# Performance work log

Hardware: AMD Instinct MI355X
Metric: run time of the kernel (lower is better)

The kernel has to match this reference:

```python
import jax, jax.numpy as jnp
import numpy as np

NUM_PTS = 1024
LATENT_SIZE = 32
BETA = 0.1


def setup_inputs() -> dict:
    key = jax.random.key(0)
    k1, k2, k3, k4 = jax.random.split(key, 4)
    B = 128
    return {
        "recon_x": jax.random.normal(k1, (B, NUM_PTS, 3), dtype=jnp.float32),
        "x": jax.random.normal(k2, (B, NUM_PTS, 3), dtype=jnp.float32),
        "mu": jax.random.normal(k3, (B, LATENT_SIZE), dtype=jnp.float32),
        "logvar": jax.random.normal(k4, (B, LATENT_SIZE), dtype=jnp.float32),
    }


def _chamfer(recon_x, x):
    # Batched squared pairwise distances: P[b, i, j] = ||x[b,i] - recon_x[b,j]||^2
    xx = jnp.sum(x * x, axis=-1)              # [B, N]
    yy = jnp.sum(recon_x * recon_x, axis=-1)  # [B, N]
    xy = jnp.einsum("bnd,bmd->bnm", x, recon_x)  # [B, N, N]
    P = xx[:, :, None] + yy[:, None, :] - 2.0 * xy
    # Bidirectional min + sum
    loss_1 = jnp.sum(jnp.min(P, axis=1))  # for each recon point, nearest x point
    loss_2 = jnp.sum(jnp.min(P, axis=2))  # for each x point, nearest recon point
    return loss_1 + loss_2


def reference(recon_x, x, mu, logvar):
    RE = _chamfer(recon_x, x) / NUM_PTS
    KLD = -0.5 * jnp.sum(1.0 + logvar - mu * mu - jnp.exp(logvar))
    KLD = KLD / LATENT_SIZE
    return RE + KLD * BETA
```

## Files before the change

### kernel.cpp

```cpp
#include <hip/hip_runtime.h>

#define NUM_PTS 1024
#define NBATCH 128
#define BT 256
#define RT 256
#define NJC 8
#define JCH 64
#define R 16
#define CHAMF_SCALE (1.0f / 1024.0f)
#define KLD_SCALE   (-0.5f * 0.1f / 32.0f)

#define WS_CHUNK (NBATCH * NUM_PTS)
#define WS_DIR   (NJC * WS_CHUNK)

__global__ __launch_bounds__(BT, 4) void chamfer_part(
    const float* __restrict__ recon_x,
    const float* __restrict__ x,
    float* __restrict__ ws)
{
    const int b  = blockIdx.x & 127;
    const int c  = blockIdx.x >> 7;
    const int w  = threadIdx.x >> 6;
    const int lt = threadIdx.x & 63;
    const int dir  = w & 1;
    const int half = w >> 1;

    __shared__ float sq[4][4][JCH];
    __shared__ float comb[2][NUM_PTS + 64];

    {
        const float* qsrc = (dir == 0 ? recon_x : x)
            + (size_t)b * NUM_PTS * 3 + (size_t)(c * 128 + half * JCH + lt) * 3;
        const float qx = qsrc[0], qy = qsrc[1], qz = qsrc[2];
        sq[w][0][lt] = qx;
        sq[w][1][lt] = qy;
        sq[w][2][lt] = qz;
        sq[w][3][lt] = fmaf(qx, qx, fmaf(qy, qy, qz * qz));
    }

    const float* rp = (dir == 0 ? x : recon_x) + (size_t)b * NUM_PTS * 3;
    float vx[R], vy[R], vz[R], m[R];
    {
        float buf[48];
        const float4* __restrict__ s4 = (const float4*)(rp + 48 * lt);
        float4* bp = (float4*)buf;
#pragma unroll
        for (int i = 0; i < 12; ++i) bp[i] = s4[i];
#pragma unroll
        for (int k = 0; k < R; ++k) {
            vx[k] = -2.0f * buf[3 * k + 0];
            vy[k] = -2.0f * buf[3 * k + 1];
            vz[k] = -2.0f * buf[3 * k + 2];
            m[k]  = 1e30f;
        }
    }

    const float4* __restrict__ qxp = (const float4*)sq[w][0];
    const float4* __restrict__ qyp = (const float4*)sq[w][1];
    const float4* __restrict__ qzp = (const float4*)sq[w][2];
    const float4* __restrict__ q2p = (const float4*)sq[w][3];
#pragma unroll 2
    for (int g = 0; g < JCH / 4; ++g) {
        const float4 qx = qxp[g];
        const float4 qy = qyp[g];
        const float4 qz = qzp[g];
        const float4 q2 = q2p[g];
#pragma unroll
        for (int r = 0; r < R; ++r) {
            const float d0 = fmaf(vx[r], qx.x, fmaf(vy[r], qy.x, fmaf(vz[r], qz.x, q2.x)));
            const float d1 = fmaf(vx[r], qx.y, fmaf(vy[r], qy.y, fmaf(vz[r], qz.y, q2.y)));
            m[r] = fminf(fminf(m[r], d0), d1);
        }
#pragma unroll
        for (int r = 0; r < R; ++r) {
            const float d2 = fmaf(vx[r], qx.z, fmaf(vy[r], qy.z, fmaf(vz[r], qz.z, q2.z)));
            const float d3 = fmaf(vx[r], qx.w, fmaf(vy[r], qy.w, fmaf(vz[r], qz.w, q2.w)));
            m[r] = fminf(fminf(m[r], d2), d3);
        }
    }

    if (half == 0) {
#pragma unroll
        for (int k = 0; k < R; ++k)
            comb[dir][17 * lt + k] = m[k];
    }
    __syncthreads();
    if (half == 1) {
        float4* dst = (float4*)(ws + (size_t)dir * WS_DIR + (size_t)c * WS_CHUNK
                                + b * NUM_PTS + 16 * lt);
#pragma unroll
        for (int k4 = 0; k4 < 4; ++k4) {
            float o[4];
#pragma unroll
            for (int i = 0; i < 4; ++i) {
                const int k = 4 * k4 + i;
                const float mm = fminf(m[k], comb[dir][17 * lt + k]);
                const float r2 = 0.25f * fmaf(vx[k], vx[k],
                                        fmaf(vy[k], vy[k], vz[k] * vz[k]));
                o[i] = r2 + mm;
            }
            dst[k4] = make_float4(o[0], o[1], o[2], o[3]);
        }
    }
}

__global__ __launch_bounds__(RT) void reduce_kernel(
    const float* __restrict__ ws,
    const float* __restrict__ mu,
    const float* __restrict__ logvar,
    float* __restrict__ out)
{
    const int gid  = blockIdx.x * RT + threadIdx.x;
    const int base = gid * 4;
    const int dir  = base >> 17;
    const int rem  = base & 131071;

    const float4* p = (const float4*)(ws + (size_t)dir * WS_DIR + rem);
    float4 mn = p[0];
#pragma unroll
    for (int c = 1; c < NJC; ++c) {
        const float4 q = p[c * (WS_CHUNK / 4)];
        mn.x = fminf(mn.x, q.x);
        mn.y = fminf(mn.y, q.y);
        mn.z = fminf(mn.z, q.z);
        mn.w = fminf(mn.w, q.w);
    }
    float v = (mn.x + mn.y + mn.z + mn.w) * CHAMF_SCALE;

    if (blockIdx.x < 16) {
        const int t = blockIdx.x * RT + threadIdx.x;
        const float lv = logvar[t];
        const float mm = mu[t];
        v += (1.0f + lv - mm * mm - expf(lv)) * KLD_SCALE;
    }

    for (int off = 32; off > 0; off >>= 1)
        v += __shfl_down(v, off, 64);

    __shared__ float red[RT / 64];
    const int lane = threadIdx.x & 63;
    const int wv   = threadIdx.x >> 6;
    if (lane == 0) red[wv] = v;
    __syncthreads();
    if (threadIdx.x == 0) {
        float sum = 0.f;
        for (int wq = 0; wq < RT / 64; ++wq) sum += red[wq];
        atomicAdd(out, sum);
    }
}

extern "C" void kernel_launch(void* const* d_in, const int* in_sizes, int n_in,
                              void* d_out, int out_size, void* d_ws, size_t ws_size,
                              hipStream_t stream) {
    const float* recon_x = (const float*)d_in[0];
    const float* x       = (const float*)d_in[1];
    const float* mu      = (const float*)d_in[2];
    const float* logvar  = (const float*)d_in[3];
    float* out = (float*)d_out;
    float* ws  = (float*)d_ws;

    (void)hipMemsetAsync(out, 0, sizeof(float), stream);

    chamfer_part<<<NBATCH * NJC, BT, 0, stream>>>(recon_x, x, ws);
    reduce_kernel<<<256, RT, 0, stream>>>(ws, mu, logvar, out);
}
```

Measured before the change: 89.09 us.

## Fuse reduction into chamfer kernel via last-block-done atomic counters

Merges the separate reduction kernel into the chamfer kernel. Each batch's eighth finishing block reduces that batch's per-chunk minima plus its KLD slice, and the last batch block sums all per-batch partials into the output. This removes a kernel launch and its gap, at the cost of threadfences, atomic counters and a tail where a single block per batch does the reduction serially.

```diff
diff --git a/kernel.cpp b/kernel.cpp
--- a/kernel.cpp
+++ b/kernel.cpp
@@ -3,7 +3,6 @@
 #define NUM_PTS 1024
 #define NBATCH 128
 #define BT 256
-#define RT 256
 #define NJC 8
 #define JCH 64
 #define R 16
@@ -12,11 +11,15 @@
 
 #define WS_CHUNK (NBATCH * NUM_PTS)
 #define WS_DIR   (NJC * WS_CHUNK)
+#define WS_PART  (2 * WS_DIR)
 
-__global__ __launch_bounds__(BT, 4) void chamfer_part(
+__global__ __launch_bounds__(BT, 4) void fused_kernel(
     const float* __restrict__ recon_x,
     const float* __restrict__ x,
-    float* __restrict__ ws)
+    const float* __restrict__ mu,
+    const float* __restrict__ logvar,
+    float* __restrict__ ws,
+    float* __restrict__ out)
 {
     const int b  = blockIdx.x & 127;
     const int c  = blockIdx.x >> 7;
@@ -25,8 +28,13 @@
     const int dir  = w & 1;
     const int half = w >> 1;
 
+    int* const cnt    = (int*)(ws + WS_PART);
+    float* const bsum = ws + WS_PART + 256;
+
     __shared__ float sq[4][4][JCH];
     __shared__ float comb[2][NUM_PTS + 64];
+    __shared__ int   sflag;
+    __shared__ float red[BT / 64];
 
     {
         const float* qsrc = (dir == 0 ? recon_x : x)
@@ -102,51 +110,61 @@
             dst[k4] = make_float4(o[0], o[1], o[2], o[3]);
         }
     }
-}
 
-__global__ __launch_bounds__(RT) void reduce_kernel(
-    const float* __restrict__ ws,
-    const float* __restrict__ mu,
-    const float* __restrict__ logvar,
-    float* __restrict__ out)
-{
-    const int gid  = blockIdx.x * RT + threadIdx.x;
-    const int base = gid * 4;
-    const int dir  = base >> 17;
-    const int rem  = base & 131071;
+    __threadfence();
+    __syncthreads();
+    if (threadIdx.x == 0) sflag = atomicAdd(&cnt[b], 1);
+    __syncthreads();
+    if (sflag != 7) return;
 
-    const float4* p = (const float4*)(ws + (size_t)dir * WS_DIR + rem);
-    float4 mn = p[0];
+    __threadfence();
+    float v = 0.0f;
 #pragma unroll
-    for (int c = 1; c < NJC; ++c) {
-        const float4 q = p[c * (WS_CHUNK / 4)];
-        mn.x = fminf(mn.x, q.x);
-        mn.y = fminf(mn.y, q.y);
-        mn.z = fminf(mn.z, q.z);
-        mn.w = fminf(mn.w, q.w);
+    for (int gsel = 0; gsel < 2; ++gsel) {
+        const int grp  = threadIdx.x + BT * gsel;
+        const int rdir = grp >> 8;
+        const int rowg = grp & 255;
+        const float4* p = (const float4*)(ws + (size_t)rdir * WS_DIR
+                                          + (size_t)b * NUM_PTS) + rowg;
+        float4 mn = p[0];
+#pragma unroll
+        for (int cc = 1; cc < NJC; ++cc) {
+            const float4 q = p[cc * (WS_CHUNK / 4)];
+            mn.x = fminf(mn.x, q.x);
+            mn.y = fminf(mn.y, q.y);
+            mn.z = fminf(mn.z, q.z);
+            mn.w = fminf(mn.w, q.w);
+        }
+        v += mn.x + mn.y + mn.z + mn.w;
     }
-    float v = (mn.x + mn.y + mn.z + mn.w) * CHAMF_SCALE;
-
-    if (blockIdx.x < 16) {
-        const int t = blockIdx.x * RT + threadIdx.x;
+    v *= CHAMF_SCALE;
+    if (threadIdx.x < 32) {
+        const int t = b * 32 + threadIdx.x;
         const float lv = logvar[t];
         const float mm = mu[t];
         v += (1.0f + lv - mm * mm - expf(lv)) * KLD_SCALE;
     }
-
     for (int off = 32; off > 0; off >>= 1)
         v += __shfl_down(v, off, 64);
-
-    __shared__ float red[RT / 64];
-    const int lane = threadIdx.x & 63;
-    const int wv   = threadIdx.x >> 6;
-    if (lane == 0) red[wv] = v;
+    if ((threadIdx.x & 63) == 0) red[threadIdx.x >> 6] = v;
     __syncthreads();
     if (threadIdx.x == 0) {
-        float sum = 0.f;
-        for (int wq = 0; wq < RT / 64; ++wq) sum += red[wq];
-        atomicAdd(out, sum);
+        float s = red[0] + red[1] + red[2] + red[3];
+        bsum[b] = s;
+        __threadfence();
+        sflag = atomicAdd(&cnt[128], 1);
     }
+    __syncthreads();
+    if (sflag != 127) return;
+
+    __threadfence();
+    float f = (threadIdx.x < 128) ? bsum[threadIdx.x] : 0.0f;
+    for (int off = 32; off > 0; off >>= 1)
+        f += __shfl_down(f, off, 64);
+    if ((threadIdx.x & 63) == 0) red[threadIdx.x >> 6] = f;
+    __syncthreads();
+    if (threadIdx.x == 0)
+        out[0] = red[0] + red[1] + red[2] + red[3];
 }
 
 extern "C" void kernel_launch(void* const* d_in, const int* in_sizes, int n_in,
@@ -159,8 +177,7 @@
     float* out = (float*)d_out;
     float* ws  = (float*)d_ws;
 
-    (void)hipMemsetAsync(out, 0, sizeof(float), stream);
+    (void)hipMemsetAsync(ws + WS_PART, 0, 1024, stream);
 
-    chamfer_part<<<NBATCH * NJC, BT, 0, stream>>>(recon_x, x, ws);
-    reduce_kernel<<<256, RT, 0, stream>>>(ws, mu, logvar, out);
+    fused_kernel<<<NBATCH * NJC, BT, 0, stream>>>(recon_x, x, mu, logvar, ws, out);
 }
```

New measurement: 209.5 us. 135% more time.
